# Performance work log

Measured on AMD Instinct MI355X. Metric: run time of the kernel, lower is better.

Reference implementation:

```python
import jax, jax.numpy as jnp
import numpy as np

B = 8192
E = 8
H = 128
NUM_CLASSES = 3
SIM_THRESHOLD = 0.8
EFF_THRESHOLD = 0.1
TARGET_TEMP = 1.0
W_LB, W_EFF, W_CONS, W_ENT, W_TEMP = 0.1, 0.05, 0.1, 0.01, 0.01


def setup_inputs() -> dict:
    key = jax.random.key(0)
    k1, k2, k3, k4 = jax.random.split(key, 4)
    logits = jax.random.normal(k1, (B, NUM_CLASSES), dtype=jnp.float32)
    targets = jax.random.randint(k2, (B,), 0, NUM_CLASSES, dtype=jnp.int64)
    raw = jax.random.uniform(k3, (B, E), dtype=jnp.float32)
    routing_probs = raw / raw.sum(axis=-1, keepdims=True)  # rows sum to 1
    input_embeddings = jax.random.uniform(k4, (B, H), dtype=jnp.float32)
    temperature = jnp.ones((1,), dtype=jnp.float32)
    return {
        "logits": logits,
        "targets": targets,
        "routing_probs": routing_probs,
        "input_embeddings": input_embeddings,
        "temperature": temperature,
    }


def _dynamo_loss(logits, routing_probs, input_embeddings, temperature, targets):
    # --- task loss: cross entropy (sentiment) ---
    logp_cls = jax.nn.log_softmax(logits, axis=-1)
    task_loss = -jnp.take_along_axis(logp_cls, targets[:, None], axis=-1).mean()

    # --- load balance: var(mean usage) / (1/E)^2 (torch.var unbiased) ---
    expert_usage = routing_probs.mean(axis=0)  # [E]
    lb_loss = W_LB * jnp.var(expert_usage, ddof=1) * (E ** 2)

    # --- efficiency: sum of probs below threshold, averaged over batch ---
    small = jnp.where(routing_probs < EFF_THRESHOLD, routing_probs, 0.0)
    eff_loss = W_EFF * small.sum(axis=-1).mean()

    # --- consistency: masked pairwise KL over similar samples ---
    nrm = input_embeddings / jnp.linalg.norm(input_embeddings, axis=-1, keepdims=True)
    sim = nrm @ nrm.T  # [B, B]
    mask = (sim > SIM_THRESHOLD) & ~jnp.eye(B, dtype=bool)
    logp = jax.nn.log_softmax(routing_probs, axis=-1)  # [B, E]
    p = jnp.exp(logp)
    a = jnp.sum(p * logp, axis=-1)  # [B], sum_e p_j log p_j
    # KL(i,j) = sum_e p_j (log p_j - log p_i) = a[j] - logp[i] . p[j]
    kl = a[None, :] - logp @ p.T  # [B, B]
    num_pairs = mask.sum()
    kl_sum = jnp.sum(jnp.where(mask, kl, 0.0))
    cons_loss = W_CONS * jnp.where(num_pairs > 0, kl_sum / jnp.maximum(num_pairs, 1), 0.0)

    # --- entropy regularization (maximize entropy of routing_probs-as-probs) ---
    eps = 1e-8
    entropy = -jnp.sum(routing_probs * jnp.log(routing_probs + eps), axis=-1)
    ent_loss = W_ENT * (-entropy.mean())

    # --- temperature regularization ---
    temp_loss = W_TEMP * jnp.mean((temperature - TARGET_TEMP) ** 2)

    return task_loss + lb_loss + eff_loss + cons_loss + ent_loss + temp_loss


def reference(logits, targets, routing_probs, input_embeddings, temperature):
    return _dynamo_loss(logits, routing_probs, input_embeddings, temperature, targets)
```

## Files before the change

### kernel.cpp

```cpp
#include <hip/hip_runtime.h>
#include <stdint.h>

#define B_SZ 8192
#define LOG8 2.0794415416798357f
#define NTILE 2080
#define NCHUNK 520

typedef __attribute__((ext_vector_type(8))) short short8;
typedef __attribute__((ext_vector_type(4))) float floatx4;

__device__ inline unsigned short f2bf(float f) {
    unsigned int u = __float_as_uint(f);
    u = (u + 0x7FFFu + ((u >> 16) & 1u)) >> 16;
    return (unsigned short)u;
}
__device__ inline float bf2f(unsigned short s) {
    return __uint_as_float(((unsigned int)s) << 16);
}
__device__ inline float wredf(float x) {
#pragma unroll
    for (int o = 32; o; o >>= 1) x += __shfl_down(x, o);
    return x;
}
__device__ inline int wredi(int x) {
#pragma unroll
    for (int o = 32; o; o >>= 1) x += __shfl_down(x, o);
    return x;
}


__global__ void prep_all(const float* __restrict__ logits,
                         const int* __restrict__ targets,
                         const float* __restrict__ routing,
                         const float* __restrict__ emb,
                         unsigned short* __restrict__ nrm,
                         unsigned short* __restrict__ nlq,
                         unsigned short* __restrict__ pb,
                         float* __restrict__ aprime,
                         float* __restrict__ prepslot) {
    __shared__ float pred[4][11];
    const int bid = blockIdx.x;
    const int lane = threadIdx.x & 63;
    const int wave = threadIdx.x >> 6;

    if (bid < 2048) {
        int row = (bid << 2) + wave;
        const float2* e2 = (const float2*)(emb + (size_t)row * 128);
        float2 v = e2[lane];
        float ss = v.x * v.x + v.y * v.y;
        ss = wredf(ss);
        ss = __shfl(ss, 0);
        float inv = rsqrtf(ss);
        ushort2 o;
        o.x = f2bf(v.x * inv);
        o.y = f2bf(v.y * inv);
        ((ushort2*)(nrm + (size_t)row * 128))[lane] = o;
        return;
    }

    int row = ((bid - 2048) << 8) + threadIdx.x;

    const float4* r4 = (const float4*)(routing + (size_t)row * 8);
    float4 va = r4[0], vb = r4[1];
    float v[8] = {va.x, va.y, va.z, va.w, vb.x, vb.y, vb.z, vb.w};

    float mx = v[0];
#pragma unroll
    for (int e = 1; e < 8; ++e) mx = fmaxf(mx, v[e]);
    float ex[8], s = 0.f;
#pragma unroll
    for (int e = 0; e < 8; ++e) { ex[e] = expf(v[e] - mx); s += ex[e]; }
    float ls = logf(s);
    float inv_s = 1.f / s;

    union { unsigned short u[8]; uint4 q; } lu, pu;
    float ap = 0.f;
#pragma unroll
    for (int e = 0; e < 8; ++e) {
        unsigned short pe = f2bf(ex[e] * inv_s);
        unsigned short le = f2bf(v[e] - mx - ls + LOG8);
        pu.u[e] = pe;
        lu.u[e] = le ^ 0x8000;
        ap += bf2f(pe) * bf2f(le);
    }
    ((uint4*)nlq)[row] = lu.q;
    ((uint4*)pb)[row] = pu.q;
    aprime[row] = ap;

    float eff = 0.f, ent = 0.f;
#pragma unroll
    for (int e = 0; e < 8; ++e) {
        if (v[e] < 0.1f) eff += v[e];
        ent += v[e] * logf(v[e] + 1e-8f);
    }

    const float* lg = logits + (size_t)row * 3;
    float a0 = lg[0], a1 = lg[1], a2 = lg[2];
    float mm = fmaxf(a0, fmaxf(a1, a2));
    float lse = mm + logf(expf(a0 - mm) + expf(a1 - mm) + expf(a2 - mm));
    int tg = targets[row];
    float tv = (tg == 0) ? a0 : ((tg == 1) ? a1 : a2);
    float task = lse - tv;

    task = wredf(task);
    eff = wredf(eff);
    ent = wredf(ent);
    float cs[8];
#pragma unroll
    for (int e = 0; e < 8; ++e) cs[e] = wredf(v[e]);

    if (lane == 0) {
        pred[wave][0] = task;
        pred[wave][1] = eff;
        pred[wave][2] = ent;
#pragma unroll
        for (int e = 0; e < 8; ++e) pred[wave][3 + e] = cs[e];
    }
    __syncthreads();
    if (threadIdx.x < 11) {
        prepslot[(bid - 2048) * 11 + threadIdx.x] =
            pred[0][threadIdx.x] + pred[1][threadIdx.x] +
            pred[2][threadIdx.x] + pred[3][threadIdx.x];
    }
}

__global__ __launch_bounds__(512, 4) void tile_sym(
    const unsigned short* __restrict__ nrm,
    const unsigned short* __restrict__ nlq,
    const unsigned short* __restrict__ pb,
    const float* __restrict__ aprime,
    float* __restrict__ klslot,
    unsigned int* __restrict__ cntslot) {
    __shared__ uint4 sh[2][128][16];

    const int t = threadIdx.x;
    const int L0 = blockIdx.x << 2;

    int bi = (int)((129.0f - sqrtf((float)(16641 - 8 * L0))) * 0.5f);
    int T = bi * 64 - ((bi * (bi - 1)) >> 1);
    while (L0 < T) { --bi; T = bi * 64 - ((bi * (bi - 1)) >> 1); }
    while (L0 >= T + (64 - bi)) { T += 64 - bi; ++bi; }
    int bj = bi + (L0 - T);

    const uint4* n4 = (const uint4*)nrm;
    const int wave = t >> 6, lane = t & 63;
    const int wr = wave >> 2, wc = wave & 3;
    const int m = lane & 15, q = lane >> 4;
    const short8 zero8 = (short8){0, 0, 0, 0, 0, 0, 0, 0};

    float klLocal = 0.f;
    int cntLocal = 0;
    int prev_bi = -1;
    uint4 bpre[4];

#pragma unroll 1
    for (int tt = 0; tt < 4; ++tt) {
        const bool diag = (bi == bj);
        const int iBase = bi << 7, jBase = bj << 7;

        if (tt == 0) {
#pragma unroll
            for (int it = 0; it < 4; ++it) {
                int cc = t + (it << 9);
                int row = cc >> 4, g = cc & 15;
                int gp = g ^ (row & 15);
                sh[0][row][gp] = n4[((size_t)(iBase + row) << 4) + g];
                sh[1][row][gp] = n4[((size_t)(jBase + row) << 4) + g];
            }
        } else {
            __syncthreads();
#pragma unroll
            for (int it = 0; it < 4; ++it) {
                int cc = t + (it << 9);
                int row = cc >> 4, g = cc & 15;
                sh[1][row][g ^ (row & 15)] = bpre[it];
            }
            if (bi != prev_bi) {
#pragma unroll
                for (int it = 0; it < 4; ++it) {
                    int cc = t + (it << 9);
                    int row = cc >> 4, g = cc & 15;
                    sh[0][row][g ^ (row & 15)] = n4[((size_t)(iBase + row) << 4) + g];
                }
            }
        }
        __syncthreads();

        int nbi = bi, nbj = bj + 1;
        if (nbj == 64) { nbi = bi + 1; nbj = nbi; }
        if (tt < 3) {
#pragma unroll
            for (int it = 0; it < 4; ++it) {
                int cc = t + (it << 9);
                int row = cc >> 4, g = cc & 15;
                bpre[it] = n4[((size_t)((nbj << 7) + row) << 4) + g];
            }
        }

        short8 crA[4], crB[2];
#pragma unroll
        for (int a = 0; a < 4; ++a) {
            int ri = iBase + (wr << 6) + (a << 4) + m;
            short8 v = zero8;
            if (q == 0) v = *(const short8*)&nlq[(size_t)ri << 3];
            else if (q == 1) { if (!diag) v = *(const short8*)&pb[(size_t)ri << 3]; }
            else if (q == 2) {
                v[1] = (short)0x3F80;
                if (!diag) v[0] = (short)f2bf(aprime[ri]);
            }
            crA[a] = v;
        }
#pragma unroll
        for (int b = 0; b < 2; ++b) {
            int cj = jBase + (wc << 5) + (b << 4) + m;
            short8 v = zero8;
            if (q == 0) v = *(const short8*)&pb[(size_t)cj << 3];
            else if (q == 1) v = *(const short8*)&nlq[(size_t)cj << 3];
            else if (q == 2) {
                v[0] = (short)0x3F80;
                v[1] = (short)f2bf(aprime[cj]);
            }
            crB[b] = v;
        }

        const unsigned short* Ab = (const unsigned short*)&sh[0][0][0];
        const unsigned short* Bb = (const unsigned short*)&sh[1][0][0];

        floatx4 simacc[4][2];
#pragma unroll
        for (int a = 0; a < 4; ++a)
#pragma unroll
            for (int b = 0; b < 2; ++b) simacc[a][b] = (floatx4){0.f, 0.f, 0.f, 0.f};

#pragma unroll
        for (int ks = 0; ks < 4; ++ks) {
            const int g = (ks << 2) + q;
            short8 af[4], bfr[2];
#pragma unroll
            for (int a = 0; a < 4; ++a) {
                int ra = (wr << 6) + (a << 4) + m;
                af[a] = *(const short8*)&Ab[(ra << 7) + ((g ^ m) << 3)];
            }
#pragma unroll
            for (int b = 0; b < 2; ++b) {
                int rb = (wc << 5) + (b << 4) + m;
                bfr[b] = *(const short8*)&Bb[(rb << 7) + ((g ^ m) << 3)];
            }
#pragma unroll
            for (int a = 0; a < 4; ++a)
#pragma unroll
                for (int b = 0; b < 2; ++b)
                    simacc[a][b] = __builtin_amdgcn_mfma_f32_16x16x32_bf16(
                        af[a], bfr[b], simacc[a][b], 0, 0, 0);
        }

#pragma unroll
        for (int a = 0; a < 4; ++a) {
            const int gRow0 = iBase + (wr << 6) + (a << 4) + (q << 2);
#pragma unroll
            for (int b = 0; b < 2; ++b) {
                const int gCol = jBase + (wc << 5) + (b << 4) + m;
                floatx4 cr = __builtin_amdgcn_mfma_f32_16x16x32_bf16(
                    crA[a], crB[b], (floatx4){0.f, 0.f, 0.f, 0.f}, 0, 0, 0);
                if (diag) {
#pragma unroll
                    for (int r = 0; r < 4; ++r) {
                        if ((simacc[a][b][r] > 0.8f) && (gRow0 + r != gCol)) {
                            klLocal += cr[r];
                            cntLocal += 1;
                        }
                    }
                } else {
#pragma unroll
                    for (int r = 0; r < 4; ++r) {
                        if (simacc[a][b][r] > 0.8f) {
                            klLocal += cr[r];
                            cntLocal += 2;
                        }
                    }
                }
            }
        }

        prev_bi = bi;
        bi = nbi;
        bj = nbj;
    }

    klLocal = wredf(klLocal);
    cntLocal = wredi(cntLocal);

    __syncthreads();
    float* redk = (float*)&sh[0][0][0];
    int* redc = (int*)(redk + 8);
    if (lane == 0) { redk[wave] = klLocal; redc[wave] = cntLocal; }
    __syncthreads();

    if (t == 0) {
        float k = 0.f;
        int c = 0;
#pragma unroll
        for (int w = 0; w < 8; ++w) { k += redk[w]; c += redc[w]; }
        klslot[blockIdx.x] = k;
        cntslot[blockIdx.x] = (unsigned int)c;
    }
}

__global__ void finalize_k(const float* __restrict__ klslot,
                           const unsigned int* __restrict__ cntslot,
                           const float* __restrict__ prepslot,
                           const float* __restrict__ temp,
                           float* __restrict__ out) {
    __shared__ float sk[4];
    __shared__ int sc[4];
    __shared__ float sp[11];
    const int t = threadIdx.x, lane = t & 63, wave = t >> 6;

    float k = 0.f;
    int c = 0;
    for (int i = t; i < NCHUNK; i += 256) { k += klslot[i]; c += (int)cntslot[i]; }
    k = wredf(k);
    c = wredi(c);
    if (lane == 0) { sk[wave] = k; sc[wave] = c; }
    if (t < 11) {
        float s = 0.f;
        for (int r = 0; r < 32; ++r) s += prepslot[r * 11 + t];
        sp[t] = s;
    }
    __syncthreads();
    if (t == 0) {
        float K = sk[0] + sk[1] + sk[2] + sk[3];
        int C = sc[0] + sc[1] + sc[2] + sc[3];
        const float invB = 1.f / (float)B_SZ;
        float task = sp[0] * invB;
        float eff = 0.05f * sp[1] * invB;
        float entl = 0.01f * sp[2] * invB;
        float cons = 0.1f * (C > 0 ? K / (float)C : 0.f);
        float u[8], mean = 0.f;
        for (int e = 0; e < 8; ++e) { u[e] = sp[3 + e] * invB; mean += u[e]; }
        mean *= 0.125f;
        float var = 0.f;
        for (int e = 0; e < 8; ++e) { float d = u[e] - mean; var += d * d; }
        var *= (1.f / 7.f);
        float lb = 0.1f * var * 64.f;
        float tt = temp[0] - 1.f;
        out[0] = task + lb + eff + cons + entl + 0.01f * tt * tt;
    }
}

extern "C" void kernel_launch(void* const* d_in, const int* in_sizes, int n_in,
                              void* d_out, int out_size, void* d_ws, size_t ws_size,
                              hipStream_t stream) {
    const float* logits = (const float*)d_in[0];
    const int* targets = (const int*)d_in[1];
    const float* routing = (const float*)d_in[2];
    const float* emb = (const float*)d_in[3];
    const float* temp = (const float*)d_in[4];

    char* ws = (char*)d_ws;
    unsigned short* nrm = (unsigned short*)ws;
    unsigned short* nlq = (unsigned short*)(ws + 2097152);
    unsigned short* pb = (unsigned short*)(ws + 2228224);
    float* aprime = (float*)(ws + 2359296);
    float* klslot = (float*)(ws + 2392064);
    unsigned int* cntslot = (unsigned int*)(ws + 2394144);
    float* prepslot = (float*)(ws + 2396224);

    prep_all<<<2080, 256, 0, stream>>>(logits, targets, routing, emb,
                                       nrm, nlq, pb, aprime, prepslot);
    tile_sym<<<NCHUNK, 512, 0, stream>>>(nrm, nlq, pb, aprime, klslot, cntslot);
    finalize_k<<<1, 256, 0, stream>>>(klslot, cntslot, prepslot, temp,
                                      (float*)d_out);
}
```

Measured before the change: 121.6 us.

## Launch one tile per block in tile_sym and consolidate prep_all blocks

The sim/KL kernel now processes a single 128x128 upper-triangle tile per block across 2080 blocks, instead of four consecutive tiles per block with register prefetch of the next B tile. This drops the intra-block serial loop and its extra syncs and gives the GPU more blocks to spread across CUs, at the cost of reloading the A tile for every tile and losing the prefetch overlap. The prep kernel is also restructured to 272 blocks of 512 threads, with each normalisation block handling four row groups, and the finalize kernel and workspace offsets are updated to match the new slot counts.

```diff
diff --git a/kernel.cpp b/kernel.cpp
--- a/kernel.cpp
+++ b/kernel.cpp
@@ -4,7 +4,6 @@
 #define B_SZ 8192
 #define LOG8 2.0794415416798357f
 #define NTILE 2080
-#define NCHUNK 520
 
 typedef __attribute__((ext_vector_type(8))) short short8;
 typedef __attribute__((ext_vector_type(4))) float floatx4;
@@ -29,36 +28,40 @@
 }
 
 
-__global__ void prep_all(const float* __restrict__ logits,
-                         const int* __restrict__ targets,
-                         const float* __restrict__ routing,
-                         const float* __restrict__ emb,
-                         unsigned short* __restrict__ nrm,
-                         unsigned short* __restrict__ nlq,
-                         unsigned short* __restrict__ pb,
-                         float* __restrict__ aprime,
-                         float* __restrict__ prepslot) {
-    __shared__ float pred[4][11];
+__global__ __launch_bounds__(512) void prep_all(
+    const float* __restrict__ logits,
+    const int* __restrict__ targets,
+    const float* __restrict__ routing,
+    const float* __restrict__ emb,
+    unsigned short* __restrict__ nrm,
+    unsigned short* __restrict__ nlq,
+    unsigned short* __restrict__ pb,
+    float* __restrict__ aprime,
+    float* __restrict__ prepslot) {
+    __shared__ float pred[8][11];
     const int bid = blockIdx.x;
     const int lane = threadIdx.x & 63;
     const int wave = threadIdx.x >> 6;
 
-    if (bid < 2048) {
-        int row = (bid << 2) + wave;
-        const float2* e2 = (const float2*)(emb + (size_t)row * 128);
-        float2 v = e2[lane];
-        float ss = v.x * v.x + v.y * v.y;
-        ss = wredf(ss);
-        ss = __shfl(ss, 0);
-        float inv = rsqrtf(ss);
-        ushort2 o;
-        o.x = f2bf(v.x * inv);
-        o.y = f2bf(v.y * inv);
-        ((ushort2*)(nrm + (size_t)row * 128))[lane] = o;
+    if (bid < 256) {
+#pragma unroll
+        for (int iter = 0; iter < 4; ++iter) {
+            int row = (((iter << 8) + bid) << 3) + wave;
+            const float2* e2 = (const float2*)(emb + (size_t)row * 128);
+            float2 v = e2[lane];
+            float ss = v.x * v.x + v.y * v.y;
+            ss = wredf(ss);
+            ss = __shfl(ss, 0);
+            float inv = rsqrtf(ss);
+            ushort2 o;
+            o.x = f2bf(v.x * inv);
+            o.y = f2bf(v.y * inv);
+            ((ushort2*)(nrm + (size_t)row * 128))[lane] = o;
+        }
         return;
     }
 
-    int row = ((bid - 2048) << 8) + threadIdx.x;
+    int row = ((bid - 256) << 9) + threadIdx.x;
 
     const float4* r4 = (const float4*)(routing + (size_t)row * 8);
     float4 va = r4[0], vb = r4[1];
@@ -118,9 +121,10 @@
     }
     __syncthreads();
     if (threadIdx.x < 11) {
-        prepslot[(bid - 2048) * 11 + threadIdx.x] =
-            pred[0][threadIdx.x] + pred[1][threadIdx.x] +
-            pred[2][threadIdx.x] + pred[3][threadIdx.x];
+        float s2 = 0.f;
+#pragma unroll
+        for (int w = 0; w < 8; ++w) s2 += pred[w][threadIdx.x];
+        prepslot[(bid - 256) * 11 + threadIdx.x] = s2;
     }
 }
 
@@ -134,157 +138,120 @@
     __shared__ uint4 sh[2][128][16];
 
     const int t = threadIdx.x;
-    const int L0 = blockIdx.x << 2;
-
-    int bi = (int)((129.0f - sqrtf((float)(16641 - 8 * L0))) * 0.5f);
+    const int L = blockIdx.x;
+
+    int bi = (int)((129.0f - sqrtf((float)(16641 - 8 * L))) * 0.5f);
     int T = bi * 64 - ((bi * (bi - 1)) >> 1);
-    while (L0 < T) { --bi; T = bi * 64 - ((bi * (bi - 1)) >> 1); }
-    while (L0 >= T + (64 - bi)) { T += 64 - bi; ++bi; }
-    int bj = bi + (L0 - T);
+    while (L < T) { --bi; T = bi * 64 - ((bi * (bi - 1)) >> 1); }
+    while (L >= T + (64 - bi)) { T += 64 - bi; ++bi; }
+    const int bj = bi + (L - T);
+    const bool diag = (bi == bj);
+    const int iBase = bi << 7, jBase = bj << 7;
 
     const uint4* n4 = (const uint4*)nrm;
+#pragma unroll
+    for (int it = 0; it < 4; ++it) {
+        int c = t + (it << 9);
+        int row = c >> 4, g = c & 15;
+        int gp = g ^ (row & 15);
+        uint4 va = n4[((size_t)(iBase + row) << 4) + g];
+        uint4 vb = n4[((size_t)(jBase + row) << 4) + g];
+        sh[0][row][gp] = va;
+        sh[1][row][gp] = vb;
+    }
+
     const int wave = t >> 6, lane = t & 63;
     const int wr = wave >> 2, wc = wave & 3;
     const int m = lane & 15, q = lane >> 4;
     const short8 zero8 = (short8){0, 0, 0, 0, 0, 0, 0, 0};
 
+    short8 crA[4], crB[2];
+#pragma unroll
+    for (int a = 0; a < 4; ++a) {
+        int ri = iBase + (wr << 6) + (a << 4) + m;
+        short8 v = zero8;
+        if (q == 0) v = *(const short8*)&nlq[(size_t)ri << 3];
+        else if (q == 1) { if (!diag) v = *(const short8*)&pb[(size_t)ri << 3]; }
+        else if (q == 2) {
+            v[1] = (short)0x3F80;
+            if (!diag) v[0] = (short)f2bf(aprime[ri]);
+        }
+        crA[a] = v;
+    }
+#pragma unroll
+    for (int b = 0; b < 2; ++b) {
+        int cj = jBase + (wc << 5) + (b << 4) + m;
+        short8 v = zero8;
+        if (q == 0) v = *(const short8*)&pb[(size_t)cj << 3];
+        else if (q == 1) v = *(const short8*)&nlq[(size_t)cj << 3];
+        else if (q == 2) {
+            v[0] = (short)0x3F80;
+            v[1] = (short)f2bf(aprime[cj]);
+        }
+        crB[b] = v;
+    }
+
+    __syncthreads();
+
+    const unsigned short* Ab = (const unsigned short*)&sh[0][0][0];
+    const unsigned short* Bb = (const unsigned short*)&sh[1][0][0];
+
+    floatx4 simacc[4][2];
+#pragma unroll
+    for (int a = 0; a < 4; ++a)
+#pragma unroll
+        for (int b = 0; b < 2; ++b) simacc[a][b] = (floatx4){0.f, 0.f, 0.f, 0.f};
+
+#pragma unroll
+    for (int ks = 0; ks < 4; ++ks) {
+        const int g = (ks << 2) + q;
+        short8 af[4], bfr[2];
+#pragma unroll
+        for (int a = 0; a < 4; ++a) {
+            int ra = (wr << 6) + (a << 4) + m;
+            af[a] = *(const short8*)&Ab[(ra << 7) + ((g ^ m) << 3)];
+        }
+#pragma unroll
+        for (int b = 0; b < 2; ++b) {
+            int rb = (wc << 5) + (b << 4) + m;
+            bfr[b] = *(const short8*)&Bb[(rb << 7) + ((g ^ m) << 3)];
+        }
+#pragma unroll
+        for (int a = 0; a < 4; ++a)
+#pragma unroll
+            for (int b = 0; b < 2; ++b)
+                simacc[a][b] = __builtin_amdgcn_mfma_f32_16x16x32_bf16(
+                    af[a], bfr[b], simacc[a][b], 0, 0, 0);
+    }
+
     float klLocal = 0.f;
     int cntLocal = 0;
-    int prev_bi = -1;
-    uint4 bpre[4];
-
-#pragma unroll 1
-    for (int tt = 0; tt < 4; ++tt) {
-        const bool diag = (bi == bj);
-        const int iBase = bi << 7, jBase = bj << 7;
-
-        if (tt == 0) {
-#pragma unroll
-            for (int it = 0; it < 4; ++it) {
-                int cc = t + (it << 9);
-                int row = cc >> 4, g = cc & 15;
-                int gp = g ^ (row & 15);
-                sh[0][row][gp] = n4[((size_t)(iBase + row) << 4) + g];
-                sh[1][row][gp] = n4[((size_t)(jBase + row) << 4) + g];
-            }
-        } else {
-            __syncthreads();
-#pragma unroll
-            for (int it = 0; it < 4; ++it) {
-                int cc = t + (it << 9);
-                int row = cc >> 4, g = cc & 15;
-                sh[1][row][g ^ (row & 15)] = bpre[it];
-            }
-            if (bi != prev_bi) {
-#pragma unroll
-                for (int it = 0; it < 4; ++it) {
-                    int cc = t + (it << 9);
-                    int row = cc >> 4, g = cc & 15;
-                    sh[0][row][g ^ (row & 15)] = n4[((size_t)(iBase + row) << 4) + g];
+#pragma unroll
+    for (int a = 0; a < 4; ++a) {
+        const int gRow0 = iBase + (wr << 6) + (a << 4) + (q << 2);
+#pragma unroll
+        for (int b = 0; b < 2; ++b) {
+            const int gCol = jBase + (wc << 5) + (b << 4) + m;
+            floatx4 cr = __builtin_amdgcn_mfma_f32_16x16x32_bf16(
+                crA[a], crB[b], (floatx4){0.f, 0.f, 0.f, 0.f}, 0, 0, 0);
+            if (diag) {
+#pragma unroll
+                for (int r = 0; r < 4; ++r) {
+                    if ((simacc[a][b][r] > 0.8f) && (gRow0 + r != gCol)) {
+                        klLocal += cr[r];
+                        cntLocal += 1;
+                    }
                 }
-            }
-        }
-        __syncthreads();
-
-        int nbi = bi, nbj = bj + 1;
-        if (nbj == 64) { nbi = bi + 1; nbj = nbi; }
-        if (tt < 3) {
-#pragma unroll
-            for (int it = 0; it < 4; ++it) {
-                int cc = t + (it << 9);
-                int row = cc >> 4, g = cc & 15;
-                bpre[it] = n4[((size_t)((nbj << 7) + row) << 4) + g];
-            }
-        }
-
-        short8 crA[4], crB[2];
-#pragma unroll
-        for (int a = 0; a < 4; ++a) {
-            int ri = iBase + (wr << 6) + (a << 4) + m;
-            short8 v = zero8;
-            if (q == 0) v = *(const short8*)&nlq[(size_t)ri << 3];
-            else if (q == 1) { if (!diag) v = *(const short8*)&pb[(size_t)ri << 3]; }
-            else if (q == 2) {
-                v[1] = (short)0x3F80;
-                if (!diag) v[0] = (short)f2bf(aprime[ri]);
-            }
-            crA[a] = v;
-        }
-#pragma unroll
-        for (int b = 0; b < 2; ++b) {
-            int cj = jBase + (wc << 5) + (b << 4) + m;
-            short8 v = zero8;
-            if (q == 0) v = *(const short8*)&pb[(size_t)cj << 3];
-            else if (q == 1) v = *(const short8*)&nlq[(size_t)cj << 3];
-            else if (q == 2) {
-                v[0] = (short)0x3F80;
-                v[1] = (short)f2bf(aprime[cj]);
-            }
-            crB[b] = v;
-        }
-
-        const unsigned short* Ab = (const unsigned short*)&sh[0][0][0];
-        const unsigned short* Bb = (const unsigned short*)&sh[1][0][0];
-
-        floatx4 simacc[4][2];
-#pragma unroll
-        for (int a = 0; a < 4; ++a)
-#pragma unroll
-            for (int b = 0; b < 2; ++b) simacc[a][b] = (floatx4){0.f, 0.f, 0.f, 0.f};
-
-#pragma unroll
-        for (int ks = 0; ks < 4; ++ks) {
-            const int g = (ks << 2) + q;
-            short8 af[4], bfr[2];
-#pragma unroll
-            for (int a = 0; a < 4; ++a) {
-                int ra = (wr << 6) + (a << 4) + m;
-                af[a] = *(const short8*)&Ab[(ra << 7) + ((g ^ m) << 3)];
-            }
-#pragma unroll
-            for (int b = 0; b < 2; ++b) {
-                int rb = (wc << 5) + (b << 4) + m;
-                bfr[b] = *(const short8*)&Bb[(rb << 7) + ((g ^ m) << 3)];
-            }
-#pragma unroll
-            for (int a = 0; a < 4; ++a)
-#pragma unroll
-                for (int b = 0; b < 2; ++b)
-                    simacc[a][b] = __builtin_amdgcn_mfma_f32_16x16x32_bf16(
-                        af[a], bfr[b], simacc[a][b], 0, 0, 0);
-        }
-
-#pragma unroll
-        for (int a = 0; a < 4; ++a) {
-            const int gRow0 = iBase + (wr << 6) + (a << 4) + (q << 2);
-#pragma unroll
-            for (int b = 0; b < 2; ++b) {
-                const int gCol = jBase + (wc << 5) + (b << 4) + m;
-                floatx4 cr = __builtin_amdgcn_mfma_f32_16x16x32_bf16(
-                    crA[a], crB[b], (floatx4){0.f, 0.f, 0.f, 0.f}, 0, 0, 0);
-                if (diag) {
-#pragma unroll
-                    for (int r = 0; r < 4; ++r) {
-                        if ((simacc[a][b][r] > 0.8f) && (gRow0 + r != gCol)) {
-                            klLocal += cr[r];
-                            cntLocal += 1;
-                        }
-                    }
-                } else {
-#pragma unroll
-                    for (int r = 0; r < 4; ++r) {
-                        if (simacc[a][b][r] > 0.8f) {
-                            klLocal += cr[r];
-                            cntLocal += 2;
-                        }
+            } else {
+#pragma unroll
+                for (int r = 0; r < 4; ++r) {
+                    if (simacc[a][b][r] > 0.8f) {
+                        klLocal += cr[r];
+                        cntLocal += 2;
                     }
                 }
             }
         }
-
-        prev_bi = bi;
-        bi = nbi;
-        bj = nbj;
     }
 
     klLocal = wredf(klLocal);
@@ -301,8 +268,8 @@
         int c = 0;
 #pragma unroll
         for (int w = 0; w < 8; ++w) { k += redk[w]; c += redc[w]; }
-        klslot[blockIdx.x] = k;
-        cntslot[blockIdx.x] = (unsigned int)c;
+        klslot[L] = k;
+        cntslot[L] = (unsigned int)c;
     }
 }
 
@@ -318,13 +285,13 @@
 
     float k = 0.f;
     int c = 0;
-    for (int i = t; i < NCHUNK; i += 256) { k += klslot[i]; c += (int)cntslot[i]; }
+    for (int i = t; i < NTILE; i += 256) { k += klslot[i]; c += (int)cntslot[i]; }
     k = wredf(k);
     c = wredi(c);
     if (lane == 0) { sk[wave] = k; sc[wave] = c; }
     if (t < 11) {
         float s = 0.f;
-        for (int r = 0; r < 32; ++r) s += prepslot[r * 11 + t];
+        for (int r = 0; r < 16; ++r) s += prepslot[r * 11 + t];
         sp[t] = s;
     }
     __syncthreads();
@@ -363,12 +330,12 @@
     unsigned short* pb = (unsigned short*)(ws + 2228224);
     float* aprime = (float*)(ws + 2359296);
     float* klslot = (float*)(ws + 2392064);
-    unsigned int* cntslot = (unsigned int*)(ws + 2394144);
-    float* prepslot = (float*)(ws + 2396224);
-
-    prep_all<<<2080, 256, 0, stream>>>(logits, targets, routing, emb,
-                                       nrm, nlq, pb, aprime, prepslot);
-    tile_sym<<<NCHUNK, 512, 0, stream>>>(nrm, nlq, pb, aprime, klslot, cntslot);
+    unsigned int* cntslot = (unsigned int*)(ws + 2400384);
+    float* prepslot = (float*)(ws + 2408704);
+
+    prep_all<<<272, 512, 0, stream>>>(logits, targets, routing, emb,
+                                      nrm, nlq, pb, aprime, prepslot);
+    tile_sym<<<NTILE, 512, 0, stream>>>(nrm, nlq, pb, aprime, klslot, cntslot);
     finalize_k<<<1, 256, 0, stream>>>(klslot, cntslot, prepslot, temp,
                                       (float*)d_out);
 }
```

New measurement: 103.2 us. 15.2% less time.
